# Kernel optimization log

Hardware: AMD Instinct MI355X
Metric: run time of the kernel (lower is better)

## Reference

```python
import jax, jax.numpy as jnp
import numpy as np
from jax import lax

K, HE, HD = 4, 96, 192  # kernel_size, hidden_enc, hidden_dec (HD == 2*HE required by z -> decoder hidden)

def _conv1d(x, W, b):
    y = lax.conv_general_dilated(x, W, (1,), 'VALID', dimension_numbers=('NCH', 'OIH', 'NCH'))
    return y + b[None, :, None]

def _maxpool1d(x, k):
    return lax.reduce_window(x, -jnp.inf, lax.max, (1, 1, k), (1, 1, k), 'VALID')

def _gru_scan(x, h0, Wi, Wh, bi, bh, emit):
    # x: (B, S, D); standard PyTorch GRU cell math
    xw = jnp.einsum('bsd,gd->sbg', x, Wi) + bi  # (S, B, 3H)
    def step(h, xw_t):
        xr, xz, xn = jnp.split(xw_t, 3, axis=-1)
        hr, hz, hn = jnp.split(h @ Wh.T + bh, 3, axis=-1)
        r = jax.nn.sigmoid(xr + hr)
        zg = jax.nn.sigmoid(xz + hz)
        n = jnp.tanh(xn + r * hn)
        h_new = (1.0 - zg) * n + zg * h
        return h_new, (h_new if emit else None)
    return lax.scan(step, h0, xw)

def _bigru(x, Wif, Whf, bif, bhf, Wib, Whb, bib, bhb, H):
    h0 = jnp.zeros((x.shape[0], H), x.dtype)
    _, of = _gru_scan(x, h0, Wif, Whf, bif, bhf, True)           # (S, B, H)
    _, ob = _gru_scan(x[:, ::-1], h0, Wib, Whb, bib, bhb, True)  # reverse direction
    return jnp.swapaxes(jnp.concatenate([of, ob[::-1]], axis=-1), 0, 1)  # (B, S, 2H)

def _forward(input, W_c1, b_c1, W_c2, b_c2, Wi_muf, Wh_muf, bi_muf, bh_muf, Wi_mub, Wh_mub, bi_mub, bh_mub, Wi_sgf, Wh_sgf, bi_sgf, bh_sgf, Wi_sgb, Wh_sgb, bi_sgb, bh_sgb, Wi_d, Wh_d, bi_d, bh_d, Wl, bl):
    T = input.shape[1]  # input: (B, T, T); input_dim == seq_len == T
    # Encoder: NodeConv (conv -> relu -> maxpool -> conv -> relu); dropout=0 -> identity
    h = jax.nn.relu(_conv1d(input, W_c1, b_c1))
    h = _maxpool1d(h, K)
    h = jax.nn.relu(_conv1d(h, W_c2, b_c2))  # (B, C, F)
    om = _bigru(h, Wi_muf, Wh_muf, bi_muf, bh_muf, Wi_mub, Wh_mub, bi_mub, bh_mub, HE)
    mu = jnp.concatenate([om[:, -1, :HE], om[:, 0, HE:]], axis=1)
    og = _bigru(h, Wi_sgf, Wh_sgf, bi_sgf, bh_sgf, Wi_sgb, Wh_sgb, bi_sgb, bh_sgb, HE)
    logvar = jnp.concatenate([og[:, -1, :HE], og[:, 0, HE:]], axis=1)
    eps = jax.random.normal(jax.random.key(42), mu.shape, mu.dtype)  # fixed-eps reparameterize
    z = mu + eps * jnp.exp(0.5 * logvar)  # (B, HD)
    # Decoder: leave-one-out per-timestep GRU recompute; hidden carried across outer steps
    base = jnp.arange(T - 1)
    def outer(h_c, i):
        idx = base + (base >= i).astype(base.dtype)  # indices skipping position i
        seq = jnp.take(input, idx, axis=1)           # (B, T-1, T)
        h_new, _ = _gru_scan(seq, h_c, Wi_d, Wh_d, bi_d, bh_d, False)
        return h_new, h_new @ Wl.T + bl
    _, outs = lax.scan(outer, z, jnp.arange(T))
    return jnp.swapaxes(outs, 0, 1), mu, logvar  # (B, T, T), (B, HD), (B, HD)

def setup_inputs():
    keys = iter(jax.random.split(jax.random.key(0), 40))
    def w(*shape):
        return jax.random.normal(next(keys), shape, jnp.float32) * 0.1
    B, D, C, F = 16, 96, 64, 20  # F = ((96-4+1)//4) - 4 + 1
    inp = {"input": jax.random.normal(next(keys), (B, D, D), jnp.float32)}
    inp["W_c1"], inp["b_c1"] = w(C, D, K), jnp.zeros((C,), jnp.float32)
    inp["W_c2"], inp["b_c2"] = w(C, C, K), jnp.zeros((C,), jnp.float32)
    for nm in ["muf", "mub", "sgf", "sgb"]:
        inp["Wi_" + nm] = w(3 * HE, F)
        inp["Wh_" + nm] = w(3 * HE, HE)
        inp["bi_" + nm] = jnp.zeros((3 * HE,), jnp.float32)
        inp["bh_" + nm] = jnp.zeros((3 * HE,), jnp.float32)
    inp["Wi_d"], inp["Wh_d"] = w(3 * HD, D), w(3 * HD, HD)
    inp["bi_d"], inp["bh_d"] = jnp.zeros((3 * HD,), jnp.float32), jnp.zeros((3 * HD,), jnp.float32)
    inp["Wl"], inp["bl"] = w(D, HD), jnp.zeros((D,), jnp.float32)
    return inp

def reference(input, W_c1, b_c1, W_c2, b_c2, Wi_muf, Wh_muf, bi_muf, bh_muf, Wi_mub, Wh_mub, bi_mub, bh_mub, Wi_sgf, Wh_sgf, bi_sgf, bh_sgf, Wi_sgb, Wh_sgb, bi_sgb, bh_sgb, Wi_d, Wh_d, bi_d, bh_d, Wl, bl):
    return _forward(input, W_c1, b_c1, W_c2, b_c2, Wi_muf, Wh_muf, bi_muf, bh_muf, Wi_mub, Wh_mub, bi_mub, bh_mub, Wi_sgf, Wh_sgf, bi_sgf, bh_sgf, Wi_sgb, Wh_sgb, bi_sgb, bh_sgb, Wi_d, Wh_d, bi_d, bh_d, Wl, bl)
```

## Files before the change

### kernel.cpp

```cpp
#include <hip/hip_runtime.h>
#include <math.h>
#include <stdint.h>


namespace {

constexpr int B  = 16;
constexpr int T  = 96;
constexpr int C  = 64;
constexpr int L1 = 93;
constexpr int LP = 23;
constexpr int F  = 20;
constexpr int HE = 96;
constexpr int GE = 288;
constexpr int HD = 192;
constexpr int GD = 576;
constexpr int SD = 95;

constexpr int WS_HENC = 0;
constexpr int WS_Z    = WS_HENC + B * C * F;
constexpr int WS_XW   = WS_Z + B * HD;
constexpr int WS_WHH  = WS_XW + B * T * GD;

constexpr int OUT_MU = B * T * T;
constexpr int OUT_LV = OUT_MU + B * HD;

typedef _Float16 half8 __attribute__((ext_vector_type(8)));
typedef _Float16 half2v __attribute__((ext_vector_type(2)));
typedef float f32x4  __attribute__((ext_vector_type(4)));

constexpr float LOG2E  = 1.4426950408889634f;
constexpr float LOG2E2 = 2.8853900817779268f;

__device__ __forceinline__ float sigmf(float x) { return 1.0f / (1.0f + expf(-x)); }

__device__ __forceinline__ float fsig2(float xp) {
  return __builtin_amdgcn_rcpf(1.0f + __builtin_amdgcn_exp2f(-xp));
}
__device__ __forceinline__ float ftanh2(float vp) {
  return fmaf(-2.0f, __builtin_amdgcn_rcpf(1.0f + __builtin_amdgcn_exp2f(vp)), 1.0f);
}

__global__ __launch_bounds__(256) void enc_conv(
    const float* __restrict__ input, const float* __restrict__ Wc1,
    const float* __restrict__ bc1, const float* __restrict__ Wc2,
    const float* __restrict__ bc2, float* __restrict__ h_enc) {
  __shared__ float xin[T * T];
  __shared__ float y1[C * L1];
  const int b = blockIdx.x;
  for (int i = threadIdx.x; i < T * T; i += 256) xin[i] = input[b * T * T + i];
  __syncthreads();
  for (int idx = threadIdx.x; idx < C * L1; idx += 256) {
    const int o = idx / L1, t = idx - o * L1;
    const float* w = Wc1 + o * (T * 4);
    float acc = bc1[o];
#pragma unroll 8
    for (int i = 0; i < T; ++i) {
      float4 wv = *reinterpret_cast<const float4*>(w + i * 4);
      const float* xp = xin + i * T + t;
      acc = fmaf(wv.x, xp[0], acc);
      acc = fmaf(wv.y, xp[1], acc);
      acc = fmaf(wv.z, xp[2], acc);
      acc = fmaf(wv.w, xp[3], acc);
    }
    y1[idx] = fmaxf(acc, 0.0f);
  }
  __syncthreads();
  float* pl = xin;
  for (int idx = threadIdx.x; idx < C * LP; idx += 256) {
    const int o = idx / LP, t = idx - o * LP;
    const float* yp = y1 + o * L1 + 4 * t;
    pl[idx] = fmaxf(fmaxf(yp[0], yp[1]), fmaxf(yp[2], yp[3]));
  }
  __syncthreads();
  for (int idx = threadIdx.x; idx < C * F; idx += 256) {
    const int o = idx / F, t = idx - o * F;
    const float* w = Wc2 + o * (C * 4);
    float acc = bc2[o];
#pragma unroll 8
    for (int i = 0; i < C; ++i) {
      float4 wv = *reinterpret_cast<const float4*>(w + i * 4);
      const float* xp = pl + i * LP + t;
      acc = fmaf(wv.x, xp[0], acc);
      acc = fmaf(wv.y, xp[1], acc);
      acc = fmaf(wv.z, xp[2], acc);
      acc = fmaf(wv.w, xp[3], acc);
    }
    h_enc[b * (C * F) + idx] = fmaxf(acc, 0.0f);
  }
}

__global__ __launch_bounds__(320) void enc_gru(
    const float* __restrict__ h_enc,
    const float* __restrict__ Wi0, const float* __restrict__ Wh0,
    const float* __restrict__ bi0, const float* __restrict__ bh0,
    const float* __restrict__ Wi1, const float* __restrict__ Wh1,
    const float* __restrict__ bi1, const float* __restrict__ bh1,
    const float* __restrict__ Wi2, const float* __restrict__ Wh2,
    const float* __restrict__ bi2, const float* __restrict__ bh2,
    const float* __restrict__ Wi3, const float* __restrict__ Wh3,
    const float* __restrict__ bi3, const float* __restrict__ bh3,
    float* __restrict__ out) {
  const int chain = blockIdx.x >> 4;
  const int b = blockIdx.x & 15;
  const float *Wi, *Wh, *bi, *bh;
  if (chain == 0)      { Wi = Wi0; Wh = Wh0; bi = bi0; bh = bh0; }
  else if (chain == 1) { Wi = Wi1; Wh = Wh1; bi = bi1; bh = bh1; }
  else if (chain == 2) { Wi = Wi2; Wh = Wh2; bi = bi2; bh = bh2; }
  else                 { Wi = Wi3; Wh = Wh3; bi = bi3; bh = bh3; }
  const bool fwd = (chain & 1) == 0;
  const int off = ((chain >> 1) ? OUT_LV : OUT_MU) + b * HD + (fwd ? 0 : HE);

  __shared__ float xall[C * F];
  __shared__ float h[HE];
  __shared__ float gx[GE], ghs[GE];

  const int tid = threadIdx.x;
  for (int i = tid; i < C * F; i += 320) xall[i] = h_enc[b * (C * F) + i];
  if (tid < HE) h[tid] = 0.0f;

  float wi[F], wh[HE], big = 0.0f, bhg = 0.0f;
  if (tid < GE) {
#pragma unroll
    for (int d = 0; d < F; ++d) wi[d] = Wi[tid * F + d];
#pragma unroll
    for (int k = 0; k < HE; ++k) wh[k] = Wh[tid * HE + k];
    big = bi[tid];
    bhg = bh[tid];
  }
  __syncthreads();

  for (int s = 0; s < C; ++s) {
    const int se = fwd ? s : (C - 1 - s);
    if (tid < GE) {
      const float* xr = xall + se * F;
      float ax = big, ah = bhg;
#pragma unroll
      for (int d = 0; d < F; ++d) ax = fmaf(wi[d], xr[d], ax);
#pragma unroll
      for (int k = 0; k < HE; ++k) ah = fmaf(wh[k], h[k], ah);
      gx[tid] = ax;
      ghs[tid] = ah;
    }
    __syncthreads();
    if (tid < HE) {
      const float r  = sigmf(gx[tid] + ghs[tid]);
      const float zg = sigmf(gx[HE + tid] + ghs[HE + tid]);
      const float n  = tanhf(fmaf(r, ghs[2 * HE + tid], gx[2 * HE + tid]));
      h[tid] = fmaf(zg, h[tid] - n, n);
    }
    __syncthreads();
  }
  if (tid < HE) out[off + tid] = h[tid];
}

__device__ __forceinline__ uint32_t rotl32(uint32_t v, int d) {
  return (v << d) | (v >> (32 - d));
}

__device__ __forceinline__ float erfinv32(float x) {
  float w = -log1pf(-x * x);
  float p;
  if (w < 5.0f) {
    w -= 2.5f;
    p = 2.81022636e-08f;
    p = fmaf(p, w, 3.43273939e-07f);
    p = fmaf(p, w, -3.5233877e-06f);
    p = fmaf(p, w, -4.39150654e-06f);
    p = fmaf(p, w, 0.00021858087f);
    p = fmaf(p, w, -0.00125372503f);
    p = fmaf(p, w, -0.00417768164f);
    p = fmaf(p, w, 0.246640727f);
    p = fmaf(p, w, 1.50140941f);
  } else {
    w = sqrtf(w) - 3.0f;
    p = -0.000200214257f;
    p = fmaf(p, w, 0.000100950558f);
    p = fmaf(p, w, 0.00134934322f);
    p = fmaf(p, w, -0.00367342844f);
    p = fmaf(p, w, 0.00573950773f);
    p = fmaf(p, w, -0.0076224613f);
    p = fmaf(p, w, 0.00943887047f);
    p = fmaf(p, w, 1.00167406f);
    p = fmaf(p, w, 2.83297682f);
  }
  return p * x;
}

__global__ __launch_bounds__(256) void z_kernel(const float* __restrict__ dout,
                                                float* __restrict__ z) {
  const int p = blockIdx.x * 256 + threadIdx.x;
  if (p >= 1536) return;
  const uint32_t ks0 = 0u, ks1 = 42u;
  const uint32_t ks2 = 0x1BD11BDAu ^ ks0 ^ ks1;
  uint32_t x0 = (uint32_t)p + ks0;
  uint32_t x1 = (uint32_t)(p + 1536) + ks1;
  x0 += x1; x1 = rotl32(x1, 13) ^ x0;
  x0 += x1; x1 = rotl32(x1, 15) ^ x0;
  x0 += x1; x1 = rotl32(x1, 26) ^ x0;
  x0 += x1; x1 = rotl32(x1, 6)  ^ x0;
  x0 += ks1; x1 += ks2 + 1u;
  x0 += x1; x1 = rotl32(x1, 17) ^ x0;
  x0 += x1; x1 = rotl32(x1, 29) ^ x0;
  x0 += x1; x1 = rotl32(x1, 16) ^ x0;
  x0 += x1; x1 = rotl32(x1, 24) ^ x0;
  x0 += ks2; x1 += ks0 + 2u;
  x0 += x1; x1 = rotl32(x1, 13) ^ x0;
  x0 += x1; x1 = rotl32(x1, 15) ^ x0;
  x0 += x1; x1 = rotl32(x1, 26) ^ x0;
  x0 += x1; x1 = rotl32(x1, 6)  ^ x0;
  x0 += ks0; x1 += ks1 + 3u;
  x0 += x1; x1 = rotl32(x1, 17) ^ x0;
  x0 += x1; x1 = rotl32(x1, 29) ^ x0;
  x0 += x1; x1 = rotl32(x1, 16) ^ x0;
  x0 += x1; x1 = rotl32(x1, 24) ^ x0;
  x0 += ks1; x1 += ks2 + 4u;
  x0 += x1; x1 = rotl32(x1, 13) ^ x0;
  x0 += x1; x1 = rotl32(x1, 15) ^ x0;
  x0 += x1; x1 = rotl32(x1, 26) ^ x0;
  x0 += x1; x1 = rotl32(x1, 6)  ^ x0;
  x0 += ks2; x1 += ks0 + 5u;

  const float* mu = dout + OUT_MU;
  const float* lv = dout + OUT_LV;
  const float lo = -0.99999994f;
#pragma unroll
  for (int half = 0; half < 2; ++half) {
    const uint32_t bits = half ? x1 : x0;
    const int e = half ? (p + 1536) : p;
    const float f = __builtin_bit_cast(float, (bits >> 9) | 0x3F800000u) - 1.0f;
    const float u = fmaxf(lo, fmaf(f, 2.0f, lo));
    const float eps = 1.41421356f * erfinv32(u);
    z[e] = fmaf(eps, expf(0.5f * lv[e]), mu[e]);
  }
}

__global__ __launch_bounds__(192) void dec_xw(const float* __restrict__ input,
                                              const float* __restrict__ Wi,
                                              const float* __restrict__ bi,
                                              const float* __restrict__ bh,
                                              float* __restrict__ XW) {
  const int br = blockIdx.x;
  __shared__ float xrow[T];
  if (threadIdx.x < T) xrow[threadIdx.x] = input[br * T + threadIdx.x];
  __syncthreads();
  for (int g = threadIdx.x; g < GD; g += 192) {
    const float* w = Wi + g * T;
    float acc = bi[g] + (g < 2 * HD ? bh[g] : 0.0f);
#pragma unroll 8
    for (int d = 0; d < T; ++d) acc = fmaf(w[d], xrow[d], acc);
    XW[br * GD + g] = acc * (g < 2 * HD ? LOG2E : LOG2E2);
  }
}

__global__ __launch_bounds__(256) void wh_to_f16(const float* __restrict__ w,
                                                 _Float16* __restrict__ o) {
  const int i = blockIdx.x * 256 + threadIdx.x;
  if (i < GD * HD)
    o[i] = (_Float16)(w[i] * (i < 2 * HD * HD ? LOG2E : LOG2E2));
}

__global__ __launch_bounds__(768, 3) void decoder(
    const float* __restrict__ XW, const _Float16* __restrict__ WhH,
    const float* __restrict__ bh, const float* __restrict__ z,
    const float* __restrict__ Wl, const float* __restrict__ bl,
    float* __restrict__ dout) {
  const int b = blockIdx.x;
  const int tid = threadIdx.x;
  const int lane = tid & 63;
  const int w = tid >> 6;
  const int col = lane & 15;
  const int g4 = lane >> 4;
  const int hidx = 16 * w + col;

  __shared__ alignas(16) _Float16 hb[2][256];
  __shared__ alignas(16) float hf[HD];

  half8 bR[6], bZ[6], bN[6];
#pragma unroll
  for (int kk = 0; kk < 6; ++kk) {
    const int ko = 32 * kk + 8 * g4;
    bR[kk] = *reinterpret_cast<const half8*>(WhH + hidx * HD + ko);
    bZ[kk] = *reinterpret_cast<const half8*>(WhH + (HD + hidx) * HD + ko);
    bN[kk] = *reinterpret_cast<const half8*>(WhH + (2 * HD + hidx) * HD + ko);
  }
  const float bhn = bh[2 * HD + hidx] * LOG2E2;

  float hold = z[b * HD + hidx];
  if (g4 == 0) hb[0][hidx] = (_Float16)hold;
  __syncthreads();

  const f32x4 kZero = {0.0f, 0.0f, 0.0f, 0.0f};
  const _Float16* hrd0 = &hb[0][8 * g4];
  _Float16* hwr0 = &hb[0][hidx];
  int cur = 0;
  const float* xwb = XW + b * T * GD;

  for (int i = 0; i < T; ++i) {
    for (int s = 0; s < SD; ++s) {
      const int rr = s + (s >= i ? 1 : 0);
      const float* xwrow = xwb + rr * GD;
      const float xr = xwrow[hidx];
      const float xz = xwrow[HD + hidx];
      const float xn = xwrow[2 * HD + hidx];

      const _Float16* hp = hrd0 + cur;
      half8 a[6];
#pragma unroll
      for (int kk = 0; kk < 6; ++kk)
        a[kk] = *reinterpret_cast<const half8*>(hp + 32 * kk);

      f32x4 aR = __builtin_amdgcn_mfma_f32_16x16x32_f16(a[0], bR[0], kZero, 0, 0, 0);
      f32x4 aZ = __builtin_amdgcn_mfma_f32_16x16x32_f16(a[0], bZ[0], kZero, 0, 0, 0);
#pragma unroll
      for (int kk = 1; kk < 6; ++kk) {
        aR = __builtin_amdgcn_mfma_f32_16x16x32_f16(a[kk], bR[kk], aR, 0, 0, 0);
        aZ = __builtin_amdgcn_mfma_f32_16x16x32_f16(a[kk], bZ[kk], aZ, 0, 0, 0);
      }

      float pn0 = 0.0f, pn1 = 0.0f;
#pragma unroll
      for (int kk = 0; kk < 6; ++kk) {
        const uint4 au = __builtin_bit_cast(uint4, a[kk]);
        const uint4 bu = __builtin_bit_cast(uint4, bN[kk]);
        pn0 = __builtin_amdgcn_fdot2(__builtin_bit_cast(half2v, au.x),
                                     __builtin_bit_cast(half2v, bu.x), pn0, false);
        pn1 = __builtin_amdgcn_fdot2(__builtin_bit_cast(half2v, au.y),
                                     __builtin_bit_cast(half2v, bu.y), pn1, false);
        pn0 = __builtin_amdgcn_fdot2(__builtin_bit_cast(half2v, au.z),
                                     __builtin_bit_cast(half2v, bu.z), pn0, false);
        pn1 = __builtin_amdgcn_fdot2(__builtin_bit_cast(half2v, au.w),
                                     __builtin_bit_cast(half2v, bu.w), pn1, false);
      }
      float pn = pn0 + pn1;
      pn += __shfl_xor(pn, 16, 64);
      pn += __shfl_xor(pn, 32, 64);

      const float r  = fsig2(xr + aR[0]);
      const float zg = fsig2(xz + aZ[0]);
      const float n  = ftanh2(fmaf(r, pn + bhn, xn));
      hold = fmaf(zg, hold - n, n);

      if (g4 == 0) {
        *(hwr0 + (cur ^ 256)) = (_Float16)hold;
        if (s == SD - 1) hf[hidx] = hold;
      }
      __syncthreads();
      cur ^= 256;
    }
    if (tid < T) {
      const float* wl = Wl + tid * HD;
      float acc = bl[tid];
#pragma unroll 8
      for (int k = 0; k < HD; ++k) acc = fmaf(wl[k], hf[k], acc);
      dout[(b * T + i) * T + tid] = acc;
    }
  }
}

}

extern "C" void kernel_launch(void* const* d_in, const int* in_sizes, int n_in,
                              void* d_out, int out_size, void* d_ws,
                              size_t ws_size, hipStream_t stream) {
  const float* input  = (const float*)d_in[0];
  const float* Wc1    = (const float*)d_in[1];
  const float* bc1    = (const float*)d_in[2];
  const float* Wc2    = (const float*)d_in[3];
  const float* bc2    = (const float*)d_in[4];
  const float* Wi_muf = (const float*)d_in[5];
  const float* Wh_muf = (const float*)d_in[6];
  const float* bi_muf = (const float*)d_in[7];
  const float* bh_muf = (const float*)d_in[8];
  const float* Wi_mub = (const float*)d_in[9];
  const float* Wh_mub = (const float*)d_in[10];
  const float* bi_mub = (const float*)d_in[11];
  const float* bh_mub = (const float*)d_in[12];
  const float* Wi_sgf = (const float*)d_in[13];
  const float* Wh_sgf = (const float*)d_in[14];
  const float* bi_sgf = (const float*)d_in[15];
  const float* bh_sgf = (const float*)d_in[16];
  const float* Wi_sgb = (const float*)d_in[17];
  const float* Wh_sgb = (const float*)d_in[18];
  const float* bi_sgb = (const float*)d_in[19];
  const float* bh_sgb = (const float*)d_in[20];
  const float* Wi_d   = (const float*)d_in[21];
  const float* Wh_d   = (const float*)d_in[22];
  const float* bi_d   = (const float*)d_in[23];
  const float* bh_d   = (const float*)d_in[24];
  const float* Wl     = (const float*)d_in[25];
  const float* bl     = (const float*)d_in[26];

  float* ws = (float*)d_ws;
  float* h_enc = ws + WS_HENC;
  float* zbuf  = ws + WS_Z;
  float* XW    = ws + WS_XW;
  _Float16* WhH = (_Float16*)(ws + WS_WHH);
  float* out = (float*)d_out;

  enc_conv<<<B, 256, 0, stream>>>(input, Wc1, bc1, Wc2, bc2, h_enc);
  enc_gru<<<64, 320, 0, stream>>>(h_enc, Wi_muf, Wh_muf, bi_muf, bh_muf,
                                  Wi_mub, Wh_mub, bi_mub, bh_mub,
                                  Wi_sgf, Wh_sgf, bi_sgf, bh_sgf,
                                  Wi_sgb, Wh_sgb, bi_sgb, bh_sgb, out);
  z_kernel<<<6, 256, 0, stream>>>(out, zbuf);
  dec_xw<<<B * T, 192, 0, stream>>>(input, Wi_d, bi_d, bh_d, XW);
  wh_to_f16<<<(GD * HD + 255) / 256, 256, 0, stream>>>(Wh_d, WhH);
  decoder<<<B, 768, 0, stream>>>(XW, WhH, bh_d, zbuf, Wl, bl, out);
}
```

Before: 7.836 ms.

## Replace decoder MFMA recurrent matvec with per-quad fdot2 and DPP reduction

The decoder GRU step previously computed the R and Z gates with 16x16x32 MFMAs, using only one output column, and the N gate with fdot2 plus cross-row shuffles. Now each hidden unit is owned by a quad of four threads, each covering 48 elements of K with packed fdot2 for all three gates. Partial sums are combined with DPP quad reductions instead of ds_swizzle-style shuffles. This removes the MFMA latency and wasted work on the serial critical path, at the cost of more VALU instructions per thread and a different LDS read pattern for h.

```diff
diff --git a/kernel.cpp b/kernel.cpp
--- a/kernel.cpp
+++ b/kernel.cpp
@@ -39,6 +39,20 @@
 }
 __device__ __forceinline__ float ftanh2(float vp) {
   return fmaf(-2.0f, __builtin_amdgcn_rcpf(1.0f + __builtin_amdgcn_exp2f(vp)), 1.0f);
+}
+
+template <int CTRL>
+__device__ __forceinline__ float dpp_add(float v) {
+  int x = __builtin_bit_cast(int, v);
+  int y = __builtin_amdgcn_update_dpp(0, x, CTRL, 0xF, 0xF, true);
+  return v + __builtin_bit_cast(float, y);
+}
+__device__ __forceinline__ float quad_reduce(float v) {
+  return dpp_add<0x4E>(dpp_add<0xB1>(v));
+}
+
+__device__ __forceinline__ float fdot2f(half2v a, half2v b, float c) {
+  return __builtin_amdgcn_fdot2(a, b, c, false);
 }
 
 __global__ __launch_bounds__(256) void enc_conv(
@@ -267,32 +281,27 @@
     float* __restrict__ dout) {
   const int b = blockIdx.x;
   const int tid = threadIdx.x;
-  const int lane = tid & 63;
-  const int w = tid >> 6;
-  const int col = lane & 15;
-  const int g4 = lane >> 4;
-  const int hidx = 16 * w + col;
+  const int hidx = tid >> 2;
+  const int j = tid & 3;
 
   __shared__ alignas(16) _Float16 hb[2][256];
   __shared__ alignas(16) float hf[HD];
 
-  half8 bR[6], bZ[6], bN[6];
+  half8 wR[6], wZ[6], wN[6];
 #pragma unroll
   for (int kk = 0; kk < 6; ++kk) {
-    const int ko = 32 * kk + 8 * g4;
-    bR[kk] = *reinterpret_cast<const half8*>(WhH + hidx * HD + ko);
-    bZ[kk] = *reinterpret_cast<const half8*>(WhH + (HD + hidx) * HD + ko);
-    bN[kk] = *reinterpret_cast<const half8*>(WhH + (2 * HD + hidx) * HD + ko);
+    const int ko = 48 * j + 8 * kk;
+    wR[kk] = *reinterpret_cast<const half8*>(WhH + hidx * HD + ko);
+    wZ[kk] = *reinterpret_cast<const half8*>(WhH + (HD + hidx) * HD + ko);
+    wN[kk] = *reinterpret_cast<const half8*>(WhH + (2 * HD + hidx) * HD + ko);
   }
   const float bhn = bh[2 * HD + hidx] * LOG2E2;
 
   float hold = z[b * HD + hidx];
-  if (g4 == 0) hb[0][hidx] = (_Float16)hold;
-  __syncthreads();
-
-  const f32x4 kZero = {0.0f, 0.0f, 0.0f, 0.0f};
-  const _Float16* hrd0 = &hb[0][8 * g4];
-  _Float16* hwr0 = &hb[0][hidx];
+  if (j == 0) hb[0][hidx] = (_Float16)hold;
+  __syncthreads();
+
+  const _Float16* hrd = &hb[0][48 * j];
   int cur = 0;
   const float* xwb = XW + b * T * GD;
 
@@ -304,45 +313,43 @@
       const float xz = xwrow[HD + hidx];
       const float xn = xwrow[2 * HD + hidx];
 
-      const _Float16* hp = hrd0 + cur;
-      half8 a[6];
+      const _Float16* hp = hrd + cur;
+      half8 hq[6];
 #pragma unroll
       for (int kk = 0; kk < 6; ++kk)
-        a[kk] = *reinterpret_cast<const half8*>(hp + 32 * kk);
-
-      f32x4 aR = __builtin_amdgcn_mfma_f32_16x16x32_f16(a[0], bR[0], kZero, 0, 0, 0);
-      f32x4 aZ = __builtin_amdgcn_mfma_f32_16x16x32_f16(a[0], bZ[0], kZero, 0, 0, 0);
-#pragma unroll
-      for (int kk = 1; kk < 6; ++kk) {
-        aR = __builtin_amdgcn_mfma_f32_16x16x32_f16(a[kk], bR[kk], aR, 0, 0, 0);
-        aZ = __builtin_amdgcn_mfma_f32_16x16x32_f16(a[kk], bZ[kk], aZ, 0, 0, 0);
+        hq[kk] = *reinterpret_cast<const half8*>(hp + 8 * kk);
+
+      float r0 = 0.f, r1 = 0.f, z0 = 0.f, z1 = 0.f, n0 = 0.f, n1 = 0.f;
+#pragma unroll
+      for (int kk = 0; kk < 6; ++kk) {
+        const uint4 hu = __builtin_bit_cast(uint4, hq[kk]);
+        const uint4 ru = __builtin_bit_cast(uint4, wR[kk]);
+        const uint4 zu = __builtin_bit_cast(uint4, wZ[kk]);
+        const uint4 nu = __builtin_bit_cast(uint4, wN[kk]);
+        r0 = fdot2f(__builtin_bit_cast(half2v, hu.x), __builtin_bit_cast(half2v, ru.x), r0);
+        r1 = fdot2f(__builtin_bit_cast(half2v, hu.y), __builtin_bit_cast(half2v, ru.y), r1);
+        r0 = fdot2f(__builtin_bit_cast(half2v, hu.z), __builtin_bit_cast(half2v, ru.z), r0);
+        r1 = fdot2f(__builtin_bit_cast(half2v, hu.w), __builtin_bit_cast(half2v, ru.w), r1);
+        z0 = fdot2f(__builtin_bit_cast(half2v, hu.x), __builtin_bit_cast(half2v, zu.x), z0);
+        z1 = fdot2f(__builtin_bit_cast(half2v, hu.y), __builtin_bit_cast(half2v, zu.y), z1);
+        z0 = fdot2f(__builtin_bit_cast(half2v, hu.z), __builtin_bit_cast(half2v, zu.z), z0);
+        z1 = fdot2f(__builtin_bit_cast(half2v, hu.w), __builtin_bit_cast(half2v, zu.w), z1);
+        n0 = fdot2f(__builtin_bit_cast(half2v, hu.x), __builtin_bit_cast(half2v, nu.x), n0);
+        n1 = fdot2f(__builtin_bit_cast(half2v, hu.y), __builtin_bit_cast(half2v, nu.y), n1);
+        n0 = fdot2f(__builtin_bit_cast(half2v, hu.z), __builtin_bit_cast(half2v, nu.z), n0);
+        n1 = fdot2f(__builtin_bit_cast(half2v, hu.w), __builtin_bit_cast(half2v, nu.w), n1);
       }
-
-      float pn0 = 0.0f, pn1 = 0.0f;
-#pragma unroll
-      for (int kk = 0; kk < 6; ++kk) {
-        const uint4 au = __builtin_bit_cast(uint4, a[kk]);
-        const uint4 bu = __builtin_bit_cast(uint4, bN[kk]);
-        pn0 = __builtin_amdgcn_fdot2(__builtin_bit_cast(half2v, au.x),
-                                     __builtin_bit_cast(half2v, bu.x), pn0, false);
-        pn1 = __builtin_amdgcn_fdot2(__builtin_bit_cast(half2v, au.y),
-                                     __builtin_bit_cast(half2v, bu.y), pn1, false);
-        pn0 = __builtin_amdgcn_fdot2(__builtin_bit_cast(half2v, au.z),
-                                     __builtin_bit_cast(half2v, bu.z), pn0, false);
-        pn1 = __builtin_amdgcn_fdot2(__builtin_bit_cast(half2v, au.w),
-                                     __builtin_bit_cast(half2v, bu.w), pn1, false);
-      }
-      float pn = pn0 + pn1;
-      pn += __shfl_xor(pn, 16, 64);
-      pn += __shfl_xor(pn, 32, 64);
-
-      const float r  = fsig2(xr + aR[0]);
-      const float zg = fsig2(xz + aZ[0]);
+      const float pr = quad_reduce(r0 + r1);
+      const float pz = quad_reduce(z0 + z1);
+      const float pn = quad_reduce(n0 + n1);
+
+      const float r  = fsig2(xr + pr);
+      const float zg = fsig2(xz + pz);
       const float n  = ftanh2(fmaf(r, pn + bhn, xn));
       hold = fmaf(zg, hold - n, n);
 
-      if (g4 == 0) {
-        *(hwr0 + (cur ^ 256)) = (_Float16)hold;
+      if (j == 0) {
+        hb[0][(cur ^ 256) + hidx] = (_Float16)hold;
         if (s == SD - 1) hf[hidx] = hold;
       }
       __syncthreads();
```

Measured after the change: 7.194 ms. -8.2%, faster.

## Process two batch rows per decoder block and compute n-gate via MFMA

Applied to the files above, without the earlier changes.

The decoder block now advances two independent batch sequences together, sharing the register-resident recurrent weights and one barrier per step across both. The n-gate product moves from fdot2 with cross-lane shuffles onto MFMA, alongside the r and z gates. The aim is to fill idle MFMA and latency slots in the serial recurrence with work from a second sequence. In exchange the grid shrinks from 16 blocks to 8 and each step holds more live registers, so per-step latency may grow.

```diff
diff --git a/kernel.cpp b/kernel.cpp
--- a/kernel.cpp
+++ b/kernel.cpp
@@ -26,7 +26,6 @@
 constexpr int OUT_LV = OUT_MU + B * HD;
 
 typedef _Float16 half8 __attribute__((ext_vector_type(8)));
-typedef _Float16 half2v __attribute__((ext_vector_type(2)));
 typedef float f32x4  __attribute__((ext_vector_type(4)));
 
 constexpr float LOG2E  = 1.4426950408889634f;
@@ -265,7 +264,7 @@
     const float* __restrict__ bh, const float* __restrict__ z,
     const float* __restrict__ Wl, const float* __restrict__ bl,
     float* __restrict__ dout) {
-  const int b = blockIdx.x;
+  const int b0 = 2 * blockIdx.x;
   const int tid = threadIdx.x;
   const int lane = tid & 63;
   const int w = tid >> 6;
@@ -273,8 +272,8 @@
   const int g4 = lane >> 4;
   const int hidx = 16 * w + col;
 
-  __shared__ alignas(16) _Float16 hb[2][256];
-  __shared__ alignas(16) float hf[HD];
+  __shared__ alignas(16) _Float16 hb[2][2][256];
+  __shared__ alignas(16) float hf[2][HD];
 
   half8 bR[6], bZ[6], bN[6];
 #pragma unroll
@@ -286,74 +285,91 @@
   }
   const float bhn = bh[2 * HD + hidx] * LOG2E2;
 
-  float hold = z[b * HD + hidx];
-  if (g4 == 0) hb[0][hidx] = (_Float16)hold;
+  float hold0 = z[b0 * HD + hidx];
+  float hold1 = z[(b0 + 1) * HD + hidx];
+  if (g4 == 0) {
+    hb[0][0][hidx] = (_Float16)hold0;
+    hb[0][1][hidx] = (_Float16)hold1;
+  }
   __syncthreads();
 
   const f32x4 kZero = {0.0f, 0.0f, 0.0f, 0.0f};
-  const _Float16* hrd0 = &hb[0][8 * g4];
-  _Float16* hwr0 = &hb[0][hidx];
+  const _Float16* hrd = &hb[0][0][8 * g4];
+  _Float16* hwr = &hb[0][0][hidx];
   int cur = 0;
-  const float* xwb = XW + b * T * GD;
+  const float* xwb0 = XW + b0 * T * GD;
+  const float* xwb1 = XW + (b0 + 1) * T * GD;
 
   for (int i = 0; i < T; ++i) {
     for (int s = 0; s < SD; ++s) {
       const int rr = s + (s >= i ? 1 : 0);
-      const float* xwrow = xwb + rr * GD;
-      const float xr = xwrow[hidx];
-      const float xz = xwrow[HD + hidx];
-      const float xn = xwrow[2 * HD + hidx];
-
-      const _Float16* hp = hrd0 + cur;
-      half8 a[6];
-#pragma unroll
-      for (int kk = 0; kk < 6; ++kk)
-        a[kk] = *reinterpret_cast<const half8*>(hp + 32 * kk);
-
-      f32x4 aR = __builtin_amdgcn_mfma_f32_16x16x32_f16(a[0], bR[0], kZero, 0, 0, 0);
-      f32x4 aZ = __builtin_amdgcn_mfma_f32_16x16x32_f16(a[0], bZ[0], kZero, 0, 0, 0);
+      const float* xwrow0 = xwb0 + rr * GD;
+      const float* xwrow1 = xwb1 + rr * GD;
+      const float xr0 = xwrow0[hidx];
+      const float xz0 = xwrow0[HD + hidx];
+      const float xn0 = xwrow0[2 * HD + hidx];
+      const float xr1 = xwrow1[hidx];
+      const float xz1 = xwrow1[HD + hidx];
+      const float xn1 = xwrow1[2 * HD + hidx];
+
+      const _Float16* hp0 = hrd + cur;
+      const _Float16* hp1 = hrd + cur + 256;
+      half8 a0[6], a1[6];
+#pragma unroll
+      for (int kk = 0; kk < 6; ++kk) {
+        a0[kk] = *reinterpret_cast<const half8*>(hp0 + 32 * kk);
+        a1[kk] = *reinterpret_cast<const half8*>(hp1 + 32 * kk);
+      }
+
+      f32x4 aR0 = __builtin_amdgcn_mfma_f32_16x16x32_f16(a0[0], bR[0], kZero, 0, 0, 0);
+      f32x4 aZ0 = __builtin_amdgcn_mfma_f32_16x16x32_f16(a0[0], bZ[0], kZero, 0, 0, 0);
+      f32x4 aN0 = __builtin_amdgcn_mfma_f32_16x16x32_f16(a0[0], bN[0], kZero, 0, 0, 0);
+      f32x4 aR1 = __builtin_amdgcn_mfma_f32_16x16x32_f16(a1[0], bR[0], kZero, 0, 0, 0);
+      f32x4 aZ1 = __builtin_amdgcn_mfma_f32_16x16x32_f16(a1[0], bZ[0], kZero, 0, 0, 0);
+      f32x4 aN1 = __builtin_amdgcn_mfma_f32_16x16x32_f16(a1[0], bN[0], kZero, 0, 0, 0);
 #pragma unroll
       for (int kk = 1; kk < 6; ++kk) {
-        aR = __builtin_amdgcn_mfma_f32_16x16x32_f16(a[kk], bR[kk], aR, 0, 0, 0);
-        aZ = __builtin_amdgcn_mfma_f32_16x16x32_f16(a[kk], bZ[kk], aZ, 0, 0, 0);
+        aR0 = __builtin_amdgcn_mfma_f32_16x16x32_f16(a0[kk], bR[kk], aR0, 0, 0, 0);
+        aZ0 = __builtin_amdgcn_mfma_f32_16x16x32_f16(a0[kk], bZ[kk], aZ0, 0, 0, 0);
+        aN0 = __builtin_amdgcn_mfma_f32_16x16x32_f16(a0[kk], bN[kk], aN0, 0, 0, 0);
+        aR1 = __builtin_amdgcn_mfma_f32_16x16x32_f16(a1[kk], bR[kk], aR1, 0, 0, 0);
+        aZ1 = __builtin_amdgcn_mfma_f32_16x16x32_f16(a1[kk], bZ[kk], aZ1, 0, 0, 0);
+        aN1 = __builtin_amdgcn_mfma_f32_16x16x32_f16(a1[kk], bN[kk], aN1, 0, 0, 0);
       }
 
-      float pn0 = 0.0f, pn1 = 0.0f;
-#pragma unroll
-      for (int kk = 0; kk < 6; ++kk) {
-        const uint4 au = __builtin_bit_cast(uint4, a[kk]);
-        const uint4 bu = __builtin_bit_cast(uint4, bN[kk]);
-        pn0 = __builtin_amdgcn_fdot2(__builtin_bit_cast(half2v, au.x),
-                                     __builtin_bit_cast(half2v, bu.x), pn0, false);
-        pn1 = __builtin_amdgcn_fdot2(__builtin_bit_cast(half2v, au.y),
-                                     __builtin_bit_cast(half2v, bu.y), pn1, false);
-        pn0 = __builtin_amdgcn_fdot2(__builtin_bit_cast(half2v, au.z),
-                                     __builtin_bit_cast(half2v, bu.z), pn0, false);
-        pn1 = __builtin_amdgcn_fdot2(__builtin_bit_cast(half2v, au.w),
-                                     __builtin_bit_cast(half2v, bu.w), pn1, false);
+      const int nxt = cur ^ 512;
+      {
+        const float r  = fsig2(xr0 + aR0[0]);
+        const float zg = fsig2(xz0 + aZ0[0]);
+        const float n  = ftanh2(fmaf(r, aN0[0] + bhn, xn0));
+        hold0 = fmaf(zg, hold0 - n, n);
       }
-      float pn = pn0 + pn1;
-      pn += __shfl_xor(pn, 16, 64);
-      pn += __shfl_xor(pn, 32, 64);
-
-      const float r  = fsig2(xr + aR[0]);
-      const float zg = fsig2(xz + aZ[0]);
-      const float n  = ftanh2(fmaf(r, pn + bhn, xn));
-      hold = fmaf(zg, hold - n, n);
-
+      {
+        const float r  = fsig2(xr1 + aR1[0]);
+        const float zg = fsig2(xz1 + aZ1[0]);
+        const float n  = ftanh2(fmaf(r, aN1[0] + bhn, xn1));
+        hold1 = fmaf(zg, hold1 - n, n);
+      }
       if (g4 == 0) {
-        *(hwr0 + (cur ^ 256)) = (_Float16)hold;
-        if (s == SD - 1) hf[hidx] = hold;
+        *(hwr + nxt) = (_Float16)hold0;
+        *(hwr + nxt + 256) = (_Float16)hold1;
+        if (s == SD - 1) {
+          hf[0][hidx] = hold0;
+          hf[1][hidx] = hold1;
+        }
       }
       __syncthreads();
-      cur ^= 256;
-    }
-    if (tid < T) {
-      const float* wl = Wl + tid * HD;
-      float acc = bl[tid];
+      cur = nxt;
+    }
+    if (tid < 2 * T) {
+      const int bloc = tid / T;
+      const int tq = tid - bloc * T;
+      const float* wl = Wl + tq * HD;
+      const float* hv = &hf[bloc][0];
+      float acc = bl[tq];
 #pragma unroll 8
-      for (int k = 0; k < HD; ++k) acc = fmaf(wl[k], hf[k], acc);
-      dout[(b * T + i) * T + tid] = acc;
+      for (int k = 0; k < HD; ++k) acc = fmaf(wl[k], hv[k], acc);
+      dout[((b0 + bloc) * T + i) * T + tq] = acc;
     }
   }
 }
@@ -406,5 +422,5 @@
   z_kernel<<<6, 256, 0, stream>>>(out, zbuf);
   dec_xw<<<B * T, 192, 0, stream>>>(input, Wi_d, bi_d, bh_d, XW);
   wh_to_f16<<<(GD * HD + 255) / 256, 256, 0, stream>>>(Wh_d, WhH);
-  decoder<<<B, 768, 0, stream>>>(XW, WhH, bh_d, zbuf, Wl, bl, out);
-}
+  decoder<<<B / 2, 768, 0, stream>>>(XW, WhH, bh_d, zbuf, Wl, bl, out);
+}
```

New measurement: 9.590 ms. 22.4% more time.
